# Optimization experiments

Measured on AMD Instinct MI355X. Metric: run time of the kernel, lower is better.

## Reference

```python
import jax, jax.numpy as jnp
import numpy as np

B, N, D, E = 4, 1024, 1024, 8
TOP_N = 2
THRESHOLD = 0.2
EPS = 1e-9
CAP_FACTOR = 2.0
MIN_EXPERT_CAPACITY = 4
H = int(D * 4 * 2 / 3)  # GEGLU hidden = 2730


def setup_inputs() -> dict:
    key = jax.random.key(0)
    ks = jax.random.split(key, 8)
    u = lambda k, shape, fan: jax.random.uniform(k, shape, jnp.float32, -1.0, 1.0) * (fan ** -0.5)
    return {
        "x": jax.random.normal(ks[0], (B, N, D), jnp.float32),
        "route_probs": jax.random.uniform(ks[1], (TOP_N, B, N), jnp.float32),
        "gate_w": u(ks[2], (D, E), D),
        "w1": u(ks[3], (E, D, 2 * H), 2 * H),
        "b1": u(ks[4], (E, 2 * H), 2 * H),
        "mult_bias": jnp.ones((E, H), jnp.float32),
        "w2": u(ks[5], (E, H, D), D),
        "b2": u(ks[6], (E, D), D),
    }


def reference(x, route_probs, gate_w, w1, b1, mult_bias, w2, b2):
    b, n, d = x.shape
    e = gate_w.shape[1]
    cap = max(min(n, int(n * CAP_FACTOR / e)), MIN_EXPERT_CAPACITY)  # 256

    # ---- top-n gating ----
    logits = jnp.einsum('bnd,de->bne', x, gate_w)
    raw_gates = jax.nn.softmax(logits, axis=-1)
    gate_vals, gate_idx = jax.lax.top_k(raw_gates, TOP_N)          # [b,n,k]
    gate_vals = jnp.moveaxis(gate_vals, -1, 0)                      # [k,b,n]
    gate_idx = jnp.moveaxis(gate_idx, -1, 0)                        # [k,b,n]
    one_hot_idx = jax.nn.one_hot(gate_idx, e, dtype=x.dtype)        # [k,b,n,e]

    denom = jnp.clip(gate_vals.sum(axis=0, keepdims=True), EPS)
    gate_vals = gate_vals / denom

    # route to expert k>0 with prob min(1, gate/threshold); expert 0 always routed
    should_route = route_probs < (gate_vals / THRESHOLD)
    should_route = should_route.at[0].set(True)
    mask = one_hot_idx * should_route[..., None].astype(x.dtype)    # [k,b,n,e]

    # exclusive cumsum over sequence dim -> position within each expert
    mask_cumsum = jnp.cumsum(mask, axis=2) - mask                   # [k,b,n,e]

    positions, masks = [], []
    prev_count = jnp.zeros((b, 1, e), x.dtype)
    for k in range(TOP_N):  # small fixed loop over top-n
        pos_e = (mask_cumsum[k] + prev_count) * mask[k]             # [b,n,e]
        mk = mask[k] * (pos_e < float(cap)).astype(x.dtype)
        prev_count = prev_count + mk.sum(axis=1, keepdims=True)
        positions.append(pos_e.sum(axis=-1))                        # [b,n]
        masks.append(mk)
    positions = jnp.stack(positions)                                # [k,b,n]
    mask = jnp.stack(masks)                                         # [k,b,n,e]

    mask_flat = mask.sum(axis=-1)                                   # [k,b,n] in {0,1}
    gates = gate_vals * mask_flat
    pos_one_hot = jax.nn.one_hot(positions.astype(jnp.int32), cap, dtype=x.dtype)  # [k,b,n,c]

    # combine tensor [b,n,e,c]; dispatch is its boolean support
    combine = jnp.einsum('kbn,kbne,kbnc->bnec', gates * mask_flat, one_hot_idx, pos_one_hot)
    dispatch = (combine > 0).astype(x.dtype)

    # ---- dispatch tokens to experts ----
    xe = jnp.einsum('bnd,bnec->ebcd', x, dispatch)                  # [e,b,c,d]

    # ---- per-expert GEGLU FFN (grouped GEMM) ----
    h = jnp.einsum('ebcd,edf->ebcf', xe, w1) + b1[:, None, None, :]
    val, gate = jnp.split(h, 2, axis=-1)
    act = jax.nn.gelu(gate, approximate=False) * val * mult_bias[:, None, None, :]
    out_e = jnp.einsum('ebch,ehd->ebcd', act, w2) + b2[:, None, None, :]

    # ---- combine ----
    out = jnp.einsum('ebcd,bnec->bnd', out_e, combine)
    return out


if __name__ == '__main__':
    inp = setup_inputs()
    o = reference(**inp)
    print(o.shape, o.dtype)
```

## Files before the change

kernel.cpp:

```cpp
#include <hip/hip_runtime.h>
#include <hip/hip_bf16.h>
#include <math.h>

#define B_ 4
#define N_ 1024
#define D_ 1024
#define E_ 8
#define H_ 2730
#define H2_ 5460
#define CAP_ 256
#define NTOK 4096
#define NSLOT 8192
#define NKT1 16
#define NKT2 43
#define NFG 22

typedef __attribute__((ext_vector_type(8))) short short8;
typedef __attribute__((ext_vector_type(4))) float f32x4;

__device__ __forceinline__ unsigned short f2bf(float f) {
    __hip_bfloat16 h = __float2bfloat16(f);
    return *reinterpret_cast<unsigned short*>(&h);
}

#define GLL16(g, l)                                                          \
    __builtin_amdgcn_global_load_lds(                                        \
        (const __attribute__((address_space(1))) void*)(g),                  \
        (__attribute__((address_space(3))) void*)(l), 16, 0, 0)


__global__ __launch_bounds__(256) void k_cvt1(const float* __restrict__ w1,
                                              unsigned short* __restrict__ w1p) {
    const int fg = blockIdx.x;
    const int kt = blockIdx.y;
    const int e  = blockIdx.z;
    const float* w1e = w1 + (size_t)e * D_ * H2_;
    unsigned short* dst = w1p + (((size_t)((e * NFG + fg) * NKT1 + kt)) << 14);
#pragma unroll
    for (int i = 0; i < 8; ++i) {
        const int o = i * 256 + threadIdx.x;
        const int l = o & 63, n16 = (o >> 6) & 15, k32 = o >> 10;
        const int f = fg * 128 + ((n16 & 7) << 4) + (l & 15);
        const int k = kt * 64 + (k32 << 5) + ((l >> 4) << 3);
        ushort4 r0 = {0, 0, 0, 0}, r1 = {0, 0, 0, 0};
        if (f < H_) {
            const float* s = w1e + (size_t)k * H2_ + (n16 >= 8 ? H_ : 0) + f;
            r0.x = f2bf(s[0]);
            r0.y = f2bf(s[(size_t)H2_]);
            r0.z = f2bf(s[(size_t)2 * H2_]);
            r0.w = f2bf(s[(size_t)3 * H2_]);
            r1.x = f2bf(s[(size_t)4 * H2_]);
            r1.y = f2bf(s[(size_t)5 * H2_]);
            r1.z = f2bf(s[(size_t)6 * H2_]);
            r1.w = f2bf(s[(size_t)7 * H2_]);
        }
        *reinterpret_cast<ushort4*>(dst + (size_t)o * 8) = r0;
        *reinterpret_cast<ushort4*>(dst + (size_t)o * 8 + 4) = r1;
    }
}

__global__ __launch_bounds__(256) void k_cvt2(const float* __restrict__ w2,
                                              unsigned short* __restrict__ w2p) {
    const int kt = blockIdx.x;
    const int nt = blockIdx.y;
    const int e  = blockIdx.z;
    const float* w2e = w2 + (size_t)e * H_ * D_;
    unsigned short* dst = w2p + (((size_t)((e * 8 + nt) * NKT2 + kt)) << 13);
#pragma unroll
    for (int i = 0; i < 4; ++i) {
        const int o = i * 256 + threadIdx.x;
        const int l = o & 63, n16 = (o >> 6) & 7, k32 = o >> 9;
        const int d = nt * 128 + (n16 << 4) + (l & 15);
        const int f = kt * 64 + (k32 << 5) + ((l >> 4) << 3);
        const float* s = w2e + (size_t)f * D_ + d;
        ushort4 r0, r1;
        r0.x = (f + 0 < H_) ? f2bf(s[0]) : 0;
        r0.y = (f + 1 < H_) ? f2bf(s[(size_t)D_]) : 0;
        r0.z = (f + 2 < H_) ? f2bf(s[(size_t)2 * D_]) : 0;
        r0.w = (f + 3 < H_) ? f2bf(s[(size_t)3 * D_]) : 0;
        r1.x = (f + 4 < H_) ? f2bf(s[(size_t)4 * D_]) : 0;
        r1.y = (f + 5 < H_) ? f2bf(s[(size_t)5 * D_]) : 0;
        r1.z = (f + 6 < H_) ? f2bf(s[(size_t)6 * D_]) : 0;
        r1.w = (f + 7 < H_) ? f2bf(s[(size_t)7 * D_]) : 0;
        *reinterpret_cast<ushort4*>(dst + (size_t)o * 8) = r0;
        *reinterpret_cast<ushort4*>(dst + (size_t)o * 8 + 4) = r1;
    }
}

__global__ __launch_bounds__(256) void k_gate(const float* __restrict__ x,
                                              const float* __restrict__ route,
                                              const float* __restrict__ gw,
                                              int* __restrict__ tokE,
                                              float* __restrict__ tokG,
                                              int* __restrict__ tokR) {
    const int wave = threadIdx.x >> 6, lane = threadIdx.x & 63;
    const int t = blockIdx.x * 4 + wave;
    float acc[E_];
#pragma unroll
    for (int e = 0; e < E_; ++e) acc[e] = 0.f;
    const float* xr = x + (size_t)t * D_;
    for (int d = lane; d < D_; d += 64) {
        float xv = xr[d];
        const float* g = gw + d * E_;
#pragma unroll
        for (int e = 0; e < E_; ++e) acc[e] = fmaf(xv, g[e], acc[e]);
    }
#pragma unroll
    for (int e = 0; e < E_; ++e) {
#pragma unroll
        for (int off = 32; off; off >>= 1) acc[e] += __shfl_xor(acc[e], off);
    }
    if (lane == 0) {
        float m = acc[0];
#pragma unroll
        for (int e = 1; e < E_; ++e) m = fmaxf(m, acc[e]);
        float p[E_]; float s = 0.f;
#pragma unroll
        for (int e = 0; e < E_; ++e) { p[e] = expf(acc[e] - m); s += p[e]; }
        int i0 = 0; float v0 = p[0];
#pragma unroll
        for (int e = 1; e < E_; ++e) if (p[e] > v0) { v0 = p[e]; i0 = e; }
        int i1 = (i0 == 0) ? 1 : 0; float v1 = p[i1];
#pragma unroll
        for (int e = 0; e < E_; ++e) if (e != i0 && p[e] > v1) { v1 = p[e]; i1 = e; }
        float p0 = v0 / s, p1 = v1 / s;
        float denom = fmaxf(p0 + p1, 1e-9f);
        float g0 = p0 / denom, g1 = p1 / denom;
        int r1 = route[NTOK + t] < (g1 / 0.2f);
        tokE[t] = i0; tokE[NTOK + t] = i1;
        tokG[t] = g0; tokG[NTOK + t] = g1;
        tokR[t] = r1;
    }
}

__global__ __launch_bounds__(256) void k_pos(const int* __restrict__ tokE,
                                             const float* __restrict__ tokG,
                                             const int* __restrict__ tokR,
                                             int* __restrict__ sot,
                                             int* __restrict__ tos) {
    const int e = blockIdx.x & 7, b = blockIdx.x >> 3;
    const int t = threadIdx.x;
    __shared__ int sc[256];
    const int base_bt = b * N_ + t * 4;
    int m0[4], m1[4];
    int c0 = 0, c1 = 0;
#pragma unroll
    for (int i = 0; i < 4; ++i) {
        int bt = base_bt + i;
        m0[i] = (tokE[bt] == e) ? 1 : 0;
        m1[i] = ((tokE[NTOK + bt] == e) && tokR[bt]) ? 1 : 0;
        c0 += m0[i]; c1 += m1[i];
    }
    int packed = c0 | (c1 << 16);
    sc[t] = packed;
    __syncthreads();
    for (int off = 1; off < 256; off <<= 1) {
        int v = (t >= off) ? sc[t - off] : 0;
        __syncthreads();
        sc[t] += v;
        __syncthreads();
    }
    int incl = sc[t];
    int total = sc[255];
    int excl = incl - packed;
    int base0 = excl & 0xffff;
    int base1 = excl >> 16;
    int kept0 = min(total & 0xffff, CAP_);
#pragma unroll
    for (int i = 0; i < 4; ++i) {
        int bt = base_bt + i;
        if (m0[i]) {
            int pos = base0++;
            if (pos < CAP_ && tokG[bt] > 0.f) {
                int s = ((e * B_ + b) << 8) + pos;
                sot[bt] = s;
                tos[s] = bt;
            }
        }
        if (m1[i]) {
            int pos = (base1++) + kept0;
            if (pos < CAP_ && tokG[NTOK + bt] > 0.f) {
                int s = ((e * B_ + b) << 8) + pos;
                sot[NTOK + bt] = s;
                tos[s] = bt;
            }
        }
    }
}

__global__ __launch_bounds__(256) void k_disp(const float* __restrict__ x,
                                              const int* __restrict__ tos,
                                              unsigned short* __restrict__ xeP) {
    const int t = threadIdx.x;
    const int s = blockIdx.x * 2 + (t >> 7);
    const int q = t & 127;
    const int bt = tos[s];
    const int kt = q >> 3, k32 = (q >> 2) & 1, kq = q & 3;
    const int lane = (kq << 4) | (s & 15);
    const int m16 = (s >> 4) & 15;
    const int sgrp = s >> 8;
    unsigned short* dst = xeP + (((size_t)(sgrp * NKT1 + kt)) << 14) + (k32 << 13) + (m16 << 9) + lane * 8;
    ushort4 r0 = {0, 0, 0, 0}, r1 = {0, 0, 0, 0};
    if (bt >= 0) {
        const float4 v0 = *reinterpret_cast<const float4*>(x + ((size_t)bt << 10) + q * 8);
        const float4 v1 = *reinterpret_cast<const float4*>(x + ((size_t)bt << 10) + q * 8 + 4);
        r0.x = f2bf(v0.x); r0.y = f2bf(v0.y); r0.z = f2bf(v0.z); r0.w = f2bf(v0.w);
        r1.x = f2bf(v1.x); r1.y = f2bf(v1.y); r1.z = f2bf(v1.z); r1.w = f2bf(v1.w);
    }
    *reinterpret_cast<ushort4*>(dst) = r0;
    *reinterpret_cast<ushort4*>(dst + 4) = r1;
}

__global__ __launch_bounds__(512) void k_ffn1(const unsigned short* __restrict__ xeP,
                                              const unsigned short* __restrict__ w1p,
                                              const float* __restrict__ b1,
                                              const float* __restrict__ mbias,
                                              unsigned short* __restrict__ actP) {
    const int wg = blockIdx.x;
    const int e = wg & 7;
    const int rem = wg >> 3;
    const int fg = rem >> 2;
    const int rt = rem & 3;
    const int sgrp = e * 4 + rt;

    __shared__ unsigned short Ab[2][16384];
    __shared__ unsigned short Bb[2][16384];

    const int tid = threadIdx.x, lane = tid & 63, w = tid >> 6;
    const int wm = w >> 2, wn = w & 3;
    const int lane8 = lane * 8;
    const int woff = w * 1024;
    const int am0 = wm * 8, bn0 = wn * 2;

    const unsigned short* abase = xeP + ((size_t)(sgrp * NKT1) << 14);
    const unsigned short* bbase = w1p + ((size_t)((e * NFG + fg) * NKT1) << 14);

    f32x4 acc[8][4];
#pragma unroll
    for (int i = 0; i < 8; ++i)
#pragma unroll
        for (int j = 0; j < 4; ++j) acc[i][j] = (f32x4)(0.f);

#define LDA1(ks, m16) (*reinterpret_cast<const short8*>(&Ab[cur][(((ks) << 4) + (m16)) * 512 + lane8]))
#define LDB1(ks, n16) (*reinterpret_cast<const short8*>(&Bb[cur][(((ks) << 4) + (n16)) * 512 + lane8]))

    {
#pragma unroll
        for (int hq = 0; hq < 2; ++hq) {
            const int off = hq * 8192 + woff;
            GLL16(abase + off + lane8, (char*)&Ab[0][off]);
            GLL16(abase + off + 512 + lane8, (char*)&Ab[0][off + 512]);
            GLL16(bbase + off + lane8, (char*)&Bb[0][off]);
            GLL16(bbase + off + 512 + lane8, (char*)&Bb[0][off + 512]);
        }
    }

    for (int kt = 0; kt < NKT1; ++kt) {
        __syncthreads();
        const int cur = kt & 1, nx = cur ^ 1;
        const bool pf = (kt + 1 < NKT1);
        const unsigned short* asn = abase + ((size_t)(kt + 1) << 14);
        const unsigned short* bsn = bbase + ((size_t)(kt + 1) << 14);
        short8 af[4], bf[4];

        if (pf) {
            const int off = woff;
            GLL16(asn + off + lane8, (char*)&Ab[nx][off]);
            GLL16(asn + off + 512 + lane8, (char*)&Ab[nx][off + 512]);
        }
        bf[0] = LDB1(0, bn0); bf[1] = LDB1(0, bn0 + 1);
        bf[2] = LDB1(0, bn0 + 8); bf[3] = LDB1(0, bn0 + 9);
        af[0] = LDA1(0, am0 + 0); af[1] = LDA1(0, am0 + 1);
        af[2] = LDA1(0, am0 + 2); af[3] = LDA1(0, am0 + 3);
        __builtin_amdgcn_s_setprio(1);
#pragma unroll
        for (int mi = 0; mi < 4; ++mi)
#pragma unroll
            for (int n = 0; n < 4; ++n)
                acc[mi][n] = __builtin_amdgcn_mfma_f32_16x16x32_bf16(af[mi], bf[n], acc[mi][n], 0, 0, 0);
        __builtin_amdgcn_s_setprio(0);

        if (pf) {
            const int off = 8192 + woff;
            GLL16(asn + off + lane8, (char*)&Ab[nx][off]);
            GLL16(asn + off + 512 + lane8, (char*)&Ab[nx][off + 512]);
        }
        af[0] = LDA1(0, am0 + 4); af[1] = LDA1(0, am0 + 5);
        af[2] = LDA1(0, am0 + 6); af[3] = LDA1(0, am0 + 7);
        __builtin_amdgcn_s_setprio(1);
#pragma unroll
        for (int mi = 0; mi < 4; ++mi)
#pragma unroll
            for (int n = 0; n < 4; ++n)
                acc[4 + mi][n] = __builtin_amdgcn_mfma_f32_16x16x32_bf16(af[mi], bf[n], acc[4 + mi][n], 0, 0, 0);
        __builtin_amdgcn_s_setprio(0);

        if (pf) {
            const int off = woff;
            GLL16(bsn + off + lane8, (char*)&Bb[nx][off]);
            GLL16(bsn + off + 512 + lane8, (char*)&Bb[nx][off + 512]);
        }
        bf[0] = LDB1(1, bn0); bf[1] = LDB1(1, bn0 + 1);
        bf[2] = LDB1(1, bn0 + 8); bf[3] = LDB1(1, bn0 + 9);
        af[0] = LDA1(1, am0 + 0); af[1] = LDA1(1, am0 + 1);
        af[2] = LDA1(1, am0 + 2); af[3] = LDA1(1, am0 + 3);
        __builtin_amdgcn_s_setprio(1);
#pragma unroll
        for (int mi = 0; mi < 4; ++mi)
#pragma unroll
            for (int n = 0; n < 4; ++n)
                acc[mi][n] = __builtin_amdgcn_mfma_f32_16x16x32_bf16(af[mi], bf[n], acc[mi][n], 0, 0, 0);
        __builtin_amdgcn_s_setprio(0);

        if (pf) {
            const int off = 8192 + woff;
            GLL16(bsn + off + lane8, (char*)&Bb[nx][off]);
            GLL16(bsn + off + 512 + lane8, (char*)&Bb[nx][off + 512]);
        }
        af[0] = LDA1(1, am0 + 4); af[1] = LDA1(1, am0 + 5);
        af[2] = LDA1(1, am0 + 6); af[3] = LDA1(1, am0 + 7);
        __builtin_amdgcn_s_setprio(1);
#pragma unroll
        for (int mi = 0; mi < 4; ++mi)
#pragma unroll
            for (int n = 0; n < 4; ++n)
                acc[4 + mi][n] = __builtin_amdgcn_mfma_f32_16x16x32_bf16(af[mi], bf[n], acc[4 + mi][n], 0, 0, 0);
        __builtin_amdgcn_s_setprio(0);
    }
#undef LDA1
#undef LDB1

    const float* b1e = b1 + (size_t)e * H2_;
    const float* mbe = mbias + (size_t)e * H_;
    const int colL = lane & 15, rq4 = (lane >> 4) * 4;
#pragma unroll
    for (int mi = 0; mi < 8; ++mi) {
        const int Rl = wm * 128 + mi * 16 + rq4;
#pragma unroll
        for (int vi = 0; vi < 2; ++vi) {
            const int f = fg * 128 + wn * 32 + vi * 16 + colL;
            if (f >= NKT2 * 64) continue;
            const bool real = f < H_;
            const float bv = real ? b1e[f] : 0.f;
            const float bg = real ? b1e[H_ + f] : 0.f;
            const float mv = real ? mbe[f] : 0.f;
            const int ktf = f >> 6, k32f = (f >> 5) & 1;
            const int lhi = ((f >> 3) & 3) << 4;
            const int bb = f & 7;
            const size_t cbase = ((size_t)(sgrp * NKT2 + ktf) << 14) + (k32f << 13);
#pragma unroll
            for (int j = 0; j < 4; ++j) {
                const int R = Rl + j;
                float a = 0.f;
                if (real) {
                    const float val = acc[mi][vi][j] + bv;
                    const float gt  = acc[mi][2 + vi][j] + bg;
                    a = 0.5f * gt * (1.f + erff(gt * 0.70710678118654752f)) * val * mv;
                }
                actP[cbase + ((R >> 4) << 9) + (size_t)((lhi | (R & 15)) * 8 + bb)] = f2bf(a);
            }
        }
    }
}

__global__ __launch_bounds__(512) void k_ffn2(const unsigned short* __restrict__ actP,
                                              const unsigned short* __restrict__ w2p,
                                              const float* __restrict__ b2,
                                              float* __restrict__ oute) {
    const int wg = blockIdx.x;
    const int e = wg & 7;
    const int rem = wg >> 3;
    const int nt = rem >> 2;
    const int mt = rem & 3;
    const int sgrp = e * 4 + mt;

    __shared__ unsigned short Ab[2][16384];
    __shared__ unsigned short Bb[2][8192];

    const int tid = threadIdx.x, lane = tid & 63, w = tid >> 6;
    const int wm = w >> 2, wn = w & 3;
    const int lane8 = lane * 8;
    const int woff = w * 1024;
    const int woffb = w * 512;
    const int am0 = wm * 8, bn0 = wn * 2;

    const unsigned short* abase = actP + ((size_t)(sgrp * NKT2) << 14);
    const unsigned short* bbase = w2p + ((size_t)((e * 8 + nt) * NKT2) << 13);

    f32x4 acc[8][2];
#pragma unroll
    for (int i = 0; i < 8; ++i)
#pragma unroll
        for (int j = 0; j < 2; ++j) acc[i][j] = (f32x4)(0.f);

#define LDA2(ks, m16) (*reinterpret_cast<const short8*>(&Ab[cur][(((ks) << 4) + (m16)) * 512 + lane8]))
#define LDB2(ks, n16) (*reinterpret_cast<const short8*>(&Bb[cur][((ks) * 8 + (n16)) * 512 + lane8]))

    {
#pragma unroll
        for (int hq = 0; hq < 2; ++hq) {
            const int off = hq * 8192 + woff;
            GLL16(abase + off + lane8, (char*)&Ab[0][off]);
            GLL16(abase + off + 512 + lane8, (char*)&Ab[0][off + 512]);
            const int boff = hq * 4096 + woffb;
            GLL16(bbase + boff + lane8, (char*)&Bb[0][boff]);
        }
    }

    for (int kt = 0; kt < NKT2; ++kt) {
        __syncthreads();
        const int cur = kt & 1, nx = cur ^ 1;
        const bool pf = (kt + 1 < NKT2);
        const unsigned short* asn = abase + ((size_t)(kt + 1) << 14);
        const unsigned short* bsn = bbase + ((size_t)(kt + 1) << 13);
        short8 af[4], bf[2];

        if (pf) {
            const int off = woff;
            GLL16(asn + off + lane8, (char*)&Ab[nx][off]);
            GLL16(asn + off + 512 + lane8, (char*)&Ab[nx][off + 512]);
        }
        bf[0] = LDB2(0, bn0); bf[1] = LDB2(0, bn0 + 1);
        af[0] = LDA2(0, am0 + 0); af[1] = LDA2(0, am0 + 1);
        af[2] = LDA2(0, am0 + 2); af[3] = LDA2(0, am0 + 3);
        __builtin_amdgcn_s_setprio(1);
#pragma unroll
        for (int mi = 0; mi < 4; ++mi)
#pragma unroll
            for (int n = 0; n < 2; ++n)
                acc[mi][n] = __builtin_amdgcn_mfma_f32_16x16x32_bf16(af[mi], bf[n], acc[mi][n], 0, 0, 0);
        __builtin_amdgcn_s_setprio(0);

        if (pf) {
            const int off = 8192 + woff;
            GLL16(asn + off + lane8, (char*)&Ab[nx][off]);
            GLL16(asn + off + 512 + lane8, (char*)&Ab[nx][off + 512]);
        }
        af[0] = LDA2(0, am0 + 4); af[1] = LDA2(0, am0 + 5);
        af[2] = LDA2(0, am0 + 6); af[3] = LDA2(0, am0 + 7);
        __builtin_amdgcn_s_setprio(1);
#pragma unroll
        for (int mi = 0; mi < 4; ++mi)
#pragma unroll
            for (int n = 0; n < 2; ++n)
                acc[4 + mi][n] = __builtin_amdgcn_mfma_f32_16x16x32_bf16(af[mi], bf[n], acc[4 + mi][n], 0, 0, 0);
        __builtin_amdgcn_s_setprio(0);

        if (pf) {
            const int boff = woffb;
            GLL16(bsn + boff + lane8, (char*)&Bb[nx][boff]);
        }
        bf[0] = LDB2(1, bn0); bf[1] = LDB2(1, bn0 + 1);
        af[0] = LDA2(1, am0 + 0); af[1] = LDA2(1, am0 + 1);
        af[2] = LDA2(1, am0 + 2); af[3] = LDA2(1, am0 + 3);
        __builtin_amdgcn_s_setprio(1);
#pragma unroll
        for (int mi = 0; mi < 4; ++mi)
#pragma unroll
            for (int n = 0; n < 2; ++n)
                acc[mi][n] = __builtin_amdgcn_mfma_f32_16x16x32_bf16(af[mi], bf[n], acc[mi][n], 0, 0, 0);
        __builtin_amdgcn_s_setprio(0);

        if (pf) {
            const int boff = 4096 + woffb;
            GLL16(bsn + boff + lane8, (char*)&Bb[nx][boff]);
        }
        af[0] = LDA2(1, am0 + 4); af[1] = LDA2(1, am0 + 5);
        af[2] = LDA2(1, am0 + 6); af[3] = LDA2(1, am0 + 7);
        __builtin_amdgcn_s_setprio(1);
#pragma unroll
        for (int mi = 0; mi < 4; ++mi)
#pragma unroll
            for (int n = 0; n < 2; ++n)
                acc[4 + mi][n] = __builtin_amdgcn_mfma_f32_16x16x32_bf16(af[mi], bf[n], acc[4 + mi][n], 0, 0, 0);
        __builtin_amdgcn_s_setprio(0);
    }
#undef LDA2
#undef LDB2

    const float* b2e = b2 + (size_t)e * D_;
    const int colL = lane & 15, rq4 = (lane >> 4) * 4;
#pragma unroll
    for (int mi = 0; mi < 8; ++mi) {
#pragma unroll
        for (int vi = 0; vi < 2; ++vi) {
            const int d = nt * 128 + wn * 32 + vi * 16 + colL;
            const float bb2 = b2e[d];
#pragma unroll
            for (int j = 0; j < 4; ++j) {
                const int R = mt * 256 + wm * 128 + mi * 16 + rq4 + j;
                oute[((size_t)(e * 1024 + R) << 10) + d] = acc[mi][vi][j] + bb2;
            }
        }
    }
}

__global__ __launch_bounds__(256) void k_comb(const float* __restrict__ oute,
                                              const int* __restrict__ sot,
                                              const float* __restrict__ tokG,
                                              float* __restrict__ out) {
    const int bt = blockIdx.x;
    const int t = threadIdx.x;
    const int s0 = sot[bt], s1 = sot[NTOK + bt];
    const float g0 = tokG[bt], g1 = tokG[NTOK + bt];
    float r0 = 0.f, r1 = 0.f, r2 = 0.f, r3 = 0.f;
    if (s0 >= 0) {
        const float4 v = *reinterpret_cast<const float4*>(oute + ((size_t)s0 << 10) + t * 4);
        r0 += g0 * v.x; r1 += g0 * v.y; r2 += g0 * v.z; r3 += g0 * v.w;
    }
    if (s1 >= 0) {
        const float4 v = *reinterpret_cast<const float4*>(oute + ((size_t)s1 << 10) + t * 4);
        r0 += g1 * v.x; r1 += g1 * v.y; r2 += g1 * v.z; r3 += g1 * v.w;
    }
    float4 o; o.x = r0; o.y = r1; o.z = r2; o.w = r3;
    *reinterpret_cast<float4*>(out + ((size_t)bt << 10) + t * 4) = o;
}

extern "C" void kernel_launch(void* const* d_in, const int* in_sizes, int n_in,
                              void* d_out, int out_size, void* d_ws, size_t ws_size,
                              hipStream_t stream) {
    const float* x     = (const float*)d_in[0];
    const float* route = (const float*)d_in[1];
    const float* gw    = (const float*)d_in[2];
    const float* w1    = (const float*)d_in[3];
    const float* b1    = (const float*)d_in[4];
    const float* mb    = (const float*)d_in[5];
    const float* w2    = (const float*)d_in[6];
    const float* b2    = (const float*)d_in[7];
    float* out = (float*)d_out;

    char* ws = (char*)d_ws;
    int*   tokE = (int*)(ws + 0);
    float* tokG = (float*)(ws + 32768);
    int*   tokR = (int*)(ws + 65536);
    int*   sot  = (int*)(ws + 81920);
    int*   tos  = (int*)(ws + 114688);
    unsigned short* xeP  = (unsigned short*)(ws + 147456);
    unsigned short* actP = (unsigned short*)(ws + 16924672);
    unsigned short* w1p  = (unsigned short*)(ws + 62013440);
    unsigned short* w2p  = (unsigned short*)(ws + 62013440);
    float* oute = (float*)(ws + 107102208);

    hipMemsetAsync(sot, 0xFF, 65536, stream);

    k_cvt1<<<dim3(NFG, NKT1, 8), 256, 0, stream>>>(w1, w1p);
    k_gate<<<NTOK / 4, 256, 0, stream>>>(x, route, gw, tokE, tokG, tokR);
    k_pos<<<E_ * B_, 256, 0, stream>>>(tokE, tokG, tokR, sot, tos);
    k_disp<<<NSLOT / 2, 256, 0, stream>>>(x, tos, xeP);
    k_ffn1<<<704, 512, 0, stream>>>(xeP, w1p, b1, mb, actP);
    k_cvt2<<<dim3(NKT2, 8, 8), 256, 0, stream>>>(w2, w2p);
    k_ffn2<<<256, 512, 0, stream>>>(actP, w2p, b2, oute);
    k_comb<<<NTOK, 256, 0, stream>>>(oute, sot, tokG, out);
}
```

Baseline: 361.3 us.

## Replace per-tile syncthreads with split vmcnt waits and mid-tile barriers in expert GEMMs

Both grouped-GEMM main loops drop the full __syncthreads at the top of each k-tile. They now wait on vmcnt for only part of the outstanding global-to-LDS loads, with one barrier at the tile start and a second barrier halfway through. Prefetch issue is reordered so the first half of the next tile's A and B lands first, which lets the first k-substep start before the second half arrives. This is meant to shorten the stall at each barrier and overlap load latency with MFMA work. The cost is that correctness now rests on hand-counted vmcnt values, which must match the number of outstanding loads.

New measurement: 370.4 us. 1.02x slower.

```diff
diff --git a/kernel.cpp b/kernel.cpp
--- a/kernel.cpp
+++ b/kernel.cpp
@@ -27,6 +27,12 @@
     __builtin_amdgcn_global_load_lds(                                        \
         (const __attribute__((address_space(1))) void*)(g),                  \
         (__attribute__((address_space(3))) void*)(l), 16, 0, 0)
+
+#define VMCNT4() asm volatile("s_waitcnt vmcnt(4)" ::: "memory")
+#define VMCNT3() asm volatile("s_waitcnt vmcnt(3)" ::: "memory")
+#define VMCNT0() asm volatile("s_waitcnt vmcnt(0)" ::: "memory")
+#define SBAR()   __builtin_amdgcn_s_barrier()
+#define SCHEDB() __builtin_amdgcn_sched_barrier(0)
 
 
 __global__ __launch_bounds__(256) void k_cvt1(const float* __restrict__ w1,
@@ -256,17 +262,17 @@
     }
 
     for (int kt = 0; kt < NKT1; ++kt) {
-        __syncthreads();
         const int cur = kt & 1, nx = cur ^ 1;
         const bool pf = (kt + 1 < NKT1);
         const unsigned short* asn = abase + ((size_t)(kt + 1) << 14);
         const unsigned short* bsn = bbase + ((size_t)(kt + 1) << 14);
         short8 af[4], bf[4];
 
-        if (pf) {
-            const int off = woff;
-            GLL16(asn + off + lane8, (char*)&Ab[nx][off]);
-            GLL16(asn + off + 512 + lane8, (char*)&Ab[nx][off + 512]);
+        SCHEDB(); VMCNT4(); SBAR(); SCHEDB();
+
+        if (pf) {
+            GLL16(asn + woff + lane8, (char*)&Ab[nx][woff]);
+            GLL16(asn + woff + 512 + lane8, (char*)&Ab[nx][woff + 512]);
         }
         bf[0] = LDB1(0, bn0); bf[1] = LDB1(0, bn0 + 1);
         bf[2] = LDB1(0, bn0 + 8); bf[3] = LDB1(0, bn0 + 9);
@@ -281,24 +287,27 @@
         __builtin_amdgcn_s_setprio(0);
 
         if (pf) {
+            GLL16(bsn + woff + lane8, (char*)&Bb[nx][woff]);
+            GLL16(bsn + woff + 512 + lane8, (char*)&Bb[nx][woff + 512]);
+        }
+        af[0] = LDA1(0, am0 + 4); af[1] = LDA1(0, am0 + 5);
+        af[2] = LDA1(0, am0 + 6); af[3] = LDA1(0, am0 + 7);
+        __builtin_amdgcn_s_setprio(1);
+#pragma unroll
+        for (int mi = 0; mi < 4; ++mi)
+#pragma unroll
+            for (int n = 0; n < 4; ++n)
+                acc[4 + mi][n] = __builtin_amdgcn_mfma_f32_16x16x32_bf16(af[mi], bf[n], acc[4 + mi][n], 0, 0, 0);
+        __builtin_amdgcn_s_setprio(0);
+
+        SCHEDB();
+        if (pf) { VMCNT4(); } else { VMCNT0(); }
+        SBAR(); SCHEDB();
+
+        if (pf) {
             const int off = 8192 + woff;
             GLL16(asn + off + lane8, (char*)&Ab[nx][off]);
             GLL16(asn + off + 512 + lane8, (char*)&Ab[nx][off + 512]);
-        }
-        af[0] = LDA1(0, am0 + 4); af[1] = LDA1(0, am0 + 5);
-        af[2] = LDA1(0, am0 + 6); af[3] = LDA1(0, am0 + 7);
-        __builtin_amdgcn_s_setprio(1);
-#pragma unroll
-        for (int mi = 0; mi < 4; ++mi)
-#pragma unroll
-            for (int n = 0; n < 4; ++n)
-                acc[4 + mi][n] = __builtin_amdgcn_mfma_f32_16x16x32_bf16(af[mi], bf[n], acc[4 + mi][n], 0, 0, 0);
-        __builtin_amdgcn_s_setprio(0);
-
-        if (pf) {
-            const int off = woff;
-            GLL16(bsn + off + lane8, (char*)&Bb[nx][off]);
-            GLL16(bsn + off + 512 + lane8, (char*)&Bb[nx][off + 512]);
         }
         bf[0] = LDB1(1, bn0); bf[1] = LDB1(1, bn0 + 1);
         bf[2] = LDB1(1, bn0 + 8); bf[3] = LDB1(1, bn0 + 9);
@@ -408,17 +417,17 @@
     }
 
     for (int kt = 0; kt < NKT2; ++kt) {
-        __syncthreads();
         const int cur = kt & 1, nx = cur ^ 1;
         const bool pf = (kt + 1 < NKT2);
         const unsigned short* asn = abase + ((size_t)(kt + 1) << 14);
         const unsigned short* bsn = bbase + ((size_t)(kt + 1) << 13);
         short8 af[4], bf[2];
 
-        if (pf) {
-            const int off = woff;
-            GLL16(asn + off + lane8, (char*)&Ab[nx][off]);
-            GLL16(asn + off + 512 + lane8, (char*)&Ab[nx][off + 512]);
+        SCHEDB(); VMCNT3(); SBAR(); SCHEDB();
+
+        if (pf) {
+            GLL16(asn + woff + lane8, (char*)&Ab[nx][woff]);
+            GLL16(asn + woff + 512 + lane8, (char*)&Ab[nx][woff + 512]);
         }
         bf[0] = LDB2(0, bn0); bf[1] = LDB2(0, bn0 + 1);
         af[0] = LDA2(0, am0 + 0); af[1] = LDA2(0, am0 + 1);
@@ -432,23 +441,26 @@
         __builtin_amdgcn_s_setprio(0);
 
         if (pf) {
+            GLL16(bsn + woffb + lane8, (char*)&Bb[nx][woffb]);
+        }
+        af[0] = LDA2(0, am0 + 4); af[1] = LDA2(0, am0 + 5);
+        af[2] = LDA2(0, am0 + 6); af[3] = LDA2(0, am0 + 7);
+        __builtin_amdgcn_s_setprio(1);
+#pragma unroll
+        for (int mi = 0; mi < 4; ++mi)
+#pragma unroll
+            for (int n = 0; n < 2; ++n)
+                acc[4 + mi][n] = __builtin_amdgcn_mfma_f32_16x16x32_bf16(af[mi], bf[n], acc[4 + mi][n], 0, 0, 0);
+        __builtin_amdgcn_s_setprio(0);
+
+        SCHEDB();
+        if (pf) { VMCNT3(); } else { VMCNT0(); }
+        SBAR(); SCHEDB();
+
+        if (pf) {
             const int off = 8192 + woff;
             GLL16(asn + off + lane8, (char*)&Ab[nx][off]);
             GLL16(asn + off + 512 + lane8, (char*)&Ab[nx][off + 512]);
-        }
-        af[0] = LDA2(0, am0 + 4); af[1] = LDA2(0, am0 + 5);
-        af[2] = LDA2(0, am0 + 6); af[3] = LDA2(0, am0 + 7);
-        __builtin_amdgcn_s_setprio(1);
-#pragma unroll
-        for (int mi = 0; mi < 4; ++mi)
-#pragma unroll
-            for (int n = 0; n < 2; ++n)
-                acc[4 + mi][n] = __builtin_amdgcn_mfma_f32_16x16x32_bf16(af[mi], bf[n], acc[4 + mi][n], 0, 0, 0);
-        __builtin_amdgcn_s_setprio(0);
-
-        if (pf) {
-            const int boff = woffb;
-            GLL16(bsn + boff + lane8, (char*)&Bb[nx][boff]);
         }
         bf[0] = LDB2(1, bn0); bf[1] = LDB2(1, bn0 + 1);
         af[0] = LDA2(1, am0 + 0); af[1] = LDA2(1, am0 + 1);
```
